# Performance work log

Hardware: AMD Instinct MI355X
Metric: run time of the kernel (lower is better)

## Reference

```python
import jax, jax.numpy as jnp
import numpy as np

B, H, W = 16, 32, 32
N = H * W
C_SEARCH, C_XCORR = 256, 64
C = C_SEARCH + C_XCORR          # phi_in_channels = gcn_in_channels
PHI_H = 64
GC_HID, GC_OUT = 128, 1
K_PTS = 48                       # keypoints per image
BN_EPS = 1e-5


def _build_coords_pair():
    # 8-neighbourhood pairs (distance^2 in {1,2}), exactly gen_8neigh_coords_pair
    idx = np.arange(N).reshape(H, W)
    ys, xs = np.meshgrid(np.arange(H), np.arange(W), indexing='ij')
    pairs8 = []
    for dy in (-1, 0, 1):
        for dx in (-1, 0, 1):
            if dy == 0 and dx == 0:
                continue
            ny, nx = ys + dy, xs + dx
            m = (ny >= 0) & (ny < H) & (nx >= 0) & (nx < W)
            pairs8.append(np.stack([idx[ys[m], xs[m]], idx[ny[m], nx[m]]], axis=1))
    pairs8 = np.concatenate(pairs8, 0)  # [7812, 2]
    # keypoint permutation pairs; keypoints on even coords -> disjoint from 8-neigh
    even = np.arange(0, H, 2)
    grid_idx = (even[:, None] * W + even[None, :]).reshape(-1)
    rng = np.random.default_rng(0)
    out = []
    for _ in range(B):
        kp = rng.choice(grid_idx, size=K_PTS, replace=False)
        a, b = np.meshgrid(kp, kp, indexing='ij')
        m = a != b
        kpairs = np.stack([a[m], b[m]], axis=1)  # K*(K-1) ordered pairs
        out.append(np.concatenate([kpairs, pairs8], 0))
    return np.stack(out, 0).astype(np.int32)  # [B, E, 2]


def setup_inputs() -> dict:
    key = jax.random.key(0)
    ks = jax.random.split(key, 10)
    u = lambda k, shape, s: jax.random.uniform(k, shape, jnp.float32, -s, s)
    inp = {
        'search_feature': jax.random.normal(ks[0], (B, C_SEARCH, H, W), jnp.float32),
        'xcorr_map': jax.random.normal(ks[1], (B, C_XCORR, H, W), jnp.float32),
        'coords_pair': jnp.asarray(_build_coords_pair()),
        # phi: Linear(C, PHI_H) + BN + ReLU, then Linear(PHI_H, 1) + Sigmoid
        'phi_w1': u(ks[2], (C, PHI_H), 1.0 / np.sqrt(C)),
        'phi_b1': u(ks[3], (PHI_H,), 1.0 / np.sqrt(C)),
        'bn_gamma': jnp.ones((PHI_H,), jnp.float32),
        'bn_beta': jnp.zeros((PHI_H,), jnp.float32),
        'phi_w2': u(ks[4], (PHI_H, 1), 1.0 / np.sqrt(PHI_H)),
        'phi_b2': u(ks[5], (1,), 1.0 / np.sqrt(PHI_H)),
        # GCN weights, torch init: uniform(-1/sqrt(out), 1/sqrt(out))
        'gc1_w': u(ks[6], (C, GC_HID), 1.0 / np.sqrt(GC_HID)),
        'gc2_w': u(ks[7], (GC_HID, GC_OUT), 1.0 / np.sqrt(GC_OUT)),
    }
    return inp


def reference(search_feature, xcorr_map, coords_pair, phi_w1, phi_b1,
              bn_gamma, bn_beta, phi_w2, phi_b2, gc1_w, gc2_w):
    # catted feature flattened: [B, C, N] (row-major h*W+w, matches torch view)
    feat = jnp.concatenate([search_feature, xcorr_map], axis=1).reshape(B, C, N)

    def per_image(f, pairs):  # f: [C, N], pairs: [E, 2]
        diff = jnp.abs(f[:, pairs[:, 0]] - f[:, pairs[:, 1]]).T  # [E, C]
        h = diff @ phi_w1 + phi_b1                                # [E, PHI_H]
        mu = jnp.mean(h, axis=0)
        var = jnp.var(h, axis=0)  # biased, as torch BN training mode
        h = (h - mu) / jnp.sqrt(var + BN_EPS) * bn_gamma + bn_beta
        h = jax.nn.relu(h)
        edge = jax.nn.sigmoid(h @ phi_w2 + phi_b2)[:, 0]          # [E]
        adj = jnp.zeros((N, N), jnp.float32).at[pairs[:, 0], pairs[:, 1]].set(edge)
        return adj

    adj = jax.vmap(per_image)(feat, coords_pair)  # [B, N, N]

    node_feat = feat.transpose(0, 2, 1)  # [B, N, C] (gcn_process_feat_xcorr=True)
    h = jax.nn.leaky_relu(jnp.einsum('bnm,bmd->bnd', adj, node_feat @ gc1_w), 0.2)
    mask = jax.nn.sigmoid(jnp.einsum('bnm,bmd->bnd', adj, h @ gc2_w))  # [B, N, 1]
    return mask[:, :, 0].reshape(B, 1, H, W)
```

## Files before the change

kernel.cpp:

```cpp
#include <hip/hip_runtime.h>
#include <hip/hip_bf16.h>
#include <hip/hip_fp16.h>

#define BB 16
#define NN 1024
#define CS 256
#define CX 64
#define CC 320
#define PH 64
#define GH 128
#define ELLW 64
#define NENG 7812
#define ROWP 324
#define RSTR 164
#define NKPH 1128
#define NGU  3906
#define NUD  5034

typedef __hip_bfloat16 bf16;
typedef __attribute__((ext_vector_type(8))) __bf16 bfrag;
typedef __attribute__((ext_vector_type(4))) float v4f;

__device__ __forceinline__ void tri_decode(int m, int& a, int& y) {
    float s = sqrtf((float)(9025 - 8 * m));
    int aa = (int)((95.0f - s) * 0.5f);
    if (aa > 0 && 47 * aa - (aa * (aa - 1)) / 2 > m) --aa;
    while (47 * (aa + 1) - ((aa + 1) * aa) / 2 <= m) ++aa;
    a = aa;
    y = aa + 1 + (m - (47 * aa - (aa * (aa - 1)) / 2));
}

__global__ __launch_bounds__(256) void k_prep_transpose(
    const float* __restrict__ search, const float* __restrict__ xcorr,
    float* __restrict__ featT,
    const float* __restrict__ w1, const float* __restrict__ gc1w,
    __bf16* __restrict__ whi, __bf16* __restrict__ wlo,
    __bf16* __restrict__ gwhi, __bf16* __restrict__ gwlo,
    int* __restrict__ cnt, float* __restrict__ Ssum, float* __restrict__ S2sum)
{
    __shared__ float tile[32][33];
    int blk = blockIdx.x;
    int tid = threadIdx.x;
    if (blk < BB * 320) {
        int b   = blk % BB;
        int rem = blk / BB;
        int ct  = rem >> 5;
        int ntl = rem & 31;
        int cl = tid >> 5, nl = tid & 31;
        const float* sb = search + (size_t)b * CS * NN;
        const float* xb = xcorr + (size_t)b * CX * NN;
        #pragma unroll
        for (int f = 0; f < 4; ++f) {
            int c = ct * 32 + cl + f * 8;
            int n = ntl * 32 + nl;
            float v = (c < CS) ? sb[(size_t)c * NN + n] : xb[(size_t)(c - CS) * NN + n];
            tile[cl + f * 8][nl] = v;
        }
        __syncthreads();
        #pragma unroll
        for (int f = 0; f < 4; ++f) {
            int nr = cl + f * 8;
            int cc = nl;
            featT[((size_t)b * NN + ntl * 32 + nr) * CC + ct * 32 + cc] = tile[cc][nr];
        }
    } else {
        int idx = (blk - BB * 320) * 256 + tid;
        if (idx < 10 * 4 * 64 * 8) {
            int j    = idx & 7;
            int lane = (idx >> 3) & 63;
            int nt   = (idx >> 9) & 3;
            int ks   = idx >> 11;
            int k = ks * 32 + (lane >> 4) * 8 + j;
            int n = nt * 16 + (lane & 15);
            float w = w1[k * PH + n];
            __bf16 h = (__bf16)w;
            whi[idx] = h;
            wlo[idx] = (__bf16)(w - (float)h);
        }
        if (idx < 10 * 8 * 64 * 8) {
            int j    = idx & 7;
            int lane = (idx >> 3) & 63;
            int nt   = (idx >> 9) & 7;
            int ks   = idx >> 12;
            int k = ks * 32 + (lane >> 4) * 8 + j;
            int n = nt * 16 + (lane & 15);
            float w = gc1w[k * GH + n];
            __bf16 h = (__bf16)w;
            gwhi[idx] = h;
            gwlo[idx] = (__bf16)(w - (float)h);
        }
        if (idx < BB * NN) cnt[idx] = 0;
        if (idx < BB * PH) { Ssum[idx] = 0.f; S2sum[idx] = 0.f; }
    }
}

__global__ __launch_bounds__(256, 2) void k_edge(
    const float* __restrict__ featT, const int* __restrict__ pairs,
    const __bf16* __restrict__ wglob, const float* __restrict__ b1,
    bf16* __restrict__ hstore, float* __restrict__ Ssum,
    float* __restrict__ S2sum, int E, int EKP)
{
    __shared__ float RowsBuf[15552];
    __shared__ int kpn[48];

    int t = threadIdx.x;
    int wave = t >> 6, lane = t & 63;
    int q = lane >> 4, r = lane & 15;
    int b = blockIdx.x % BB;
    int y = blockIdx.x / BB;

    if (t < 48) kpn[t] = pairs[((size_t)b * E + t * 47) * 2];

    const bfrag* WH = (const bfrag*)wglob;
    const bfrag* WL = WH + 2560;

    float b1v[4];
    #pragma unroll
    for (int nt = 0; nt < 4; ++nt) b1v[nt] = b1[nt * 16 + r];
    float ps[4], ps2[4];
    #pragma unroll
    for (int nt = 0; nt < 4; ++nt) { ps[nt] = 0.f; ps2[nt] = 0.f; }

    const int dyT[4] = {-1,-1,-1, 0};
    const int dxT[4] = {-1, 0, 1,-1};
    const int pfT4[4] = {0, 961, 1953, 2914};

    int d = wave;
    int dy = dyT[d], dx = dxT[d];
    int y0 = dy < 0 ? 1 : 0;
    int x0 = dx < 0 ? 1 : 0;
    int ww = (dx == 0) ? 32 : 31;
    int pfF = pfT4[d];

    const float* rowI[2];
    const float* rowJ[2];
    #pragma unroll
    for (int mt = 0; mt < 2; ++mt) {
        int x  = (mt << 4) + r;
        int ni = 32 + x;
        int xj = x + dx; xj = xj < 0 ? 0 : (xj > 31 ? 31 : xj);
        int nj = (1 + dy) * 32 + xj;
        rowI[mt] = &RowsBuf[ni * RSTR + q * 8];
        rowJ[mt] = &RowsBuf[nj * RSTR + q * 8];
    }

    v4f acc[2][4];
    #pragma unroll
    for (int mt = 0; mt < 2; ++mt)
        #pragma unroll
        for (int nt = 0; nt < 4; ++nt) acc[mt][nt] = (v4f)0.f;

    #pragma unroll
    for (int ph = 0; ph < 2; ++ph) {
        __syncthreads();
        const int ch0 = ph * 160;
        #pragma unroll
        for (int k = 0; k < 10; ++k) {
            int uu = t + k * 256;
            int node = uu / 40, c4 = uu - node * 40;
            int gy = y - 1 + (node >> 5);
            if (gy >= 0) {
                int gn = gy * 32 + (node & 31);
                float4 v = *(const float4*)&featT[((size_t)b * NN + gn) * CC
                                                  + ch0 + c4 * 4];
                *(float4*)&RowsBuf[node * RSTR + c4 * 4] = v;
            }
        }
        __syncthreads();

        const int ksBeg = ph * 5;
        #pragma unroll
        for (int ks = ksBeg; ks < ksBeg + 5; ++ks) {
            int lc = ks * 32 - ch0;
            #pragma unroll
            for (int mt = 0; mt < 2; ++mt) {
                float4 fi0 = *(const float4*)(rowI[mt] + lc);
                float4 fi1 = *(const float4*)(rowI[mt] + lc + 4);
                float4 fj0 = *(const float4*)(rowJ[mt] + lc);
                float4 fj1 = *(const float4*)(rowJ[mt] + lc + 4);
                float df[8];
                df[0] = fabsf(fi0.x - fj0.x); df[1] = fabsf(fi0.y - fj0.y);
                df[2] = fabsf(fi0.z - fj0.z); df[3] = fabsf(fi0.w - fj0.w);
                df[4] = fabsf(fi1.x - fj1.x); df[5] = fabsf(fi1.y - fj1.y);
                df[6] = fabsf(fi1.z - fj1.z); df[7] = fabsf(fi1.w - fj1.w);

                bfrag ah, al;
                #pragma unroll
                for (int kk = 0; kk < 8; ++kk) {
                    __bf16 h = (__bf16)df[kk];
                    ah[kk] = h;
                    al[kk] = (__bf16)(df[kk] - (float)h);
                }
                #pragma unroll
                for (int nt = 0; nt < 4; ++nt) {
                    bfrag bh = WH[((ks * 4 + nt) << 6) + lane];
                    bfrag bl = WL[((ks * 4 + nt) << 6) + lane];
                    acc[mt][nt] = __builtin_amdgcn_mfma_f32_16x16x32_bf16(
                        ah, bh, acc[mt][nt], 0, 0, 0);
                    acc[mt][nt] = __builtin_amdgcn_mfma_f32_16x16x32_bf16(
                        ah, bl, acc[mt][nt], 0, 0, 0);
                    acc[mt][nt] = __builtin_amdgcn_mfma_f32_16x16x32_bf16(
                        al, bh, acc[mt][nt], 0, 0, 0);
                }
            }
        }
    }

    __syncthreads();
    {
        const float4* src = (const float4*)featT;
        #pragma unroll
        for (int k = 0; k < 15; ++k) {
            int idx = t + k * 256;
            int slot = idx / 80, c4 = idx - slot * 80;
            float4 v = src[((size_t)b * NN + kpn[slot]) * 80 + c4];
            *(float4*)&RowsBuf[slot * ROWP + c4 * 4] = v;
        }
    }

    #pragma unroll
    for (int mt = 0; mt < 2; ++mt) {
        #pragma unroll
        for (int reg = 0; reg < 4; ++reg) {
            int xi = (mt << 4) + q * 4 + reg;
            int y2 = y + dy, x2 = xi + dx;
            bool valid = ((unsigned)y2 < 32u) && ((unsigned)x2 < 32u);
            if (valid) {
                int e1 = EKP + pfF + (y - y0) * ww + (xi - x0);
                bf16* h1 = hstore + ((size_t)b * E + e1) * PH + r;
                #pragma unroll
                for (int nt = 0; nt < 4; ++nt) {
                    float v = acc[mt][nt][reg] + b1v[nt];
                    h1[nt * 16] = __float2bfloat16(v);
                    ps[nt] += v;
                    ps2[nt] = fmaf(v, v, ps2[nt]);
                }
            }
        }
    }

    __syncthreads();

    int u = y + 32 * wave;
    if (u < 71) {
        int mA = u * 16 + r;
        if (mA >= NKPH) mA = NKPH - 1;
        int aI, yI;
        tri_decode(mA, aI, yI);
        const float* rI = &RowsBuf[aI * ROWP + q * 8];
        const float* rJ = &RowsBuf[yI * ROWP + q * 8];

        v4f acc2[4];
        #pragma unroll
        for (int nt = 0; nt < 4; ++nt) acc2[nt] = (v4f)0.f;

        #pragma unroll
        for (int ks = 0; ks < 10; ++ks) {
            float4 fi0 = *(const float4*)(rI + ks * 32);
            float4 fi1 = *(const float4*)(rI + ks * 32 + 4);
            float4 fj0 = *(const float4*)(rJ + ks * 32);
            float4 fj1 = *(const float4*)(rJ + ks * 32 + 4);
            float df[8];
            df[0] = fabsf(fi0.x - fj0.x); df[1] = fabsf(fi0.y - fj0.y);
            df[2] = fabsf(fi0.z - fj0.z); df[3] = fabsf(fi0.w - fj0.w);
            df[4] = fabsf(fi1.x - fj1.x); df[5] = fabsf(fi1.y - fj1.y);
            df[6] = fabsf(fi1.z - fj1.z); df[7] = fabsf(fi1.w - fj1.w);

            bfrag ah, al;
            #pragma unroll
            for (int kk = 0; kk < 8; ++kk) {
                __bf16 h = (__bf16)df[kk];
                ah[kk] = h;
                al[kk] = (__bf16)(df[kk] - (float)h);
            }
            #pragma unroll
            for (int nt = 0; nt < 4; ++nt) {
                bfrag bh = WH[((ks * 4 + nt) << 6) + lane];
                bfrag bl = WL[((ks * 4 + nt) << 6) + lane];
                acc2[nt] = __builtin_amdgcn_mfma_f32_16x16x32_bf16(ah, bh, acc2[nt], 0, 0, 0);
                acc2[nt] = __builtin_amdgcn_mfma_f32_16x16x32_bf16(ah, bl, acc2[nt], 0, 0, 0);
                acc2[nt] = __builtin_amdgcn_mfma_f32_16x16x32_bf16(al, bh, acc2[nt], 0, 0, 0);
            }
        }

        #pragma unroll
        for (int reg = 0; reg < 4; ++reg) {
            int mC = u * 16 + q * 4 + reg;
            if (mC < NKPH) {
                int a, yk;
                tri_decode(mC, a, yk);
                int e1 = a * 47 + yk - 1;
                bf16* h1 = hstore + ((size_t)b * E + e1) * PH + r;
                #pragma unroll
                for (int nt = 0; nt < 4; ++nt) {
                    float v = acc2[nt][reg] + b1v[nt];
                    h1[nt * 16] = __float2bfloat16(v);
                    ps[nt] += v;
                    ps2[nt] = fmaf(v, v, ps2[nt]);
                }
            }
        }
    }

    __syncthreads();
    float* sS  = RowsBuf;
    float* sS2 = RowsBuf + PH;
    if (t < PH) { sS[t] = 0.f; sS2[t] = 0.f; }
    __syncthreads();
    #pragma unroll
    for (int nt = 0; nt < 4; ++nt) {
        float p1 = ps[nt]  + __shfl_xor(ps[nt], 16, 64);
        p1 += __shfl_xor(p1, 32, 64);
        float p2 = ps2[nt] + __shfl_xor(ps2[nt], 16, 64);
        p2 += __shfl_xor(p2, 32, 64);
        if (lane < 16) {
            atomicAdd(&sS[nt * 16 + r],  2.0f * p1);
            atomicAdd(&sS2[nt * 16 + r], 2.0f * p2);
        }
    }
    __syncthreads();
    if (t < PH) {
        atomicAdd(&Ssum[b * PH + t],  sS[t]);
        atomicAdd(&S2sum[b * PH + t], sS2[t]);
    }
}

__global__ __launch_bounds__(256, 2) void k_val_gc1(
    const float* __restrict__ featT, const __bf16* __restrict__ gwhi,
    const __bf16* __restrict__ gwlo, __half* __restrict__ g1,
    const bf16* __restrict__ hstore, const float* __restrict__ Ssum,
    const float* __restrict__ S2sum, const float* __restrict__ gamma,
    const float* __restrict__ beta, const float* __restrict__ w2,
    const float* __restrict__ b2, const int* __restrict__ pairs,
    int* __restrict__ cnt, int* __restrict__ ecol, float* __restrict__ eval_,
    int E, int EKP, int nGC)
{
    __shared__ ushort WG[40960];

    int t = threadIdx.x;
    if ((int)blockIdx.x < nGC) {
        int b = blockIdx.x % BB;
        int rem = blockIdx.x / BB;
        int half = rem & 1;
        int m0 = b * NN + (rem >> 1) * 64;

        {
            uint4* dst = (uint4*)WG;
            const uint4* sh = (const uint4*)gwhi;
            const uint4* sl = (const uint4*)gwlo;
            #pragma unroll
            for (int k = 0; k < 10; ++k) {
                int u = t + k * 256;
                int chunk = u >> 6, v = u & 63;
                int ks = chunk >> 2, ntp = chunk & 3;
                int src = (ks * 8 + half * 4 + ntp) * 64 + v;
                dst[u]        = sh[src];
                dst[2560 + u] = sl[src];
            }
        }

        int wave = t >> 6, lane = t & 63;
        int q = lane >> 4, r = lane & 15;
        const float* fp = featT + (size_t)(m0 + wave * 16 + r) * CC + q * 8;

        float fa[2][8];
        auto LOADA = [&](int ks, int buf) {
            const float4* p = (const float4*)(fp + ks * 32);
            *(float4*)&fa[buf][0] = p[0];
            *(float4*)&fa[buf][4] = p[1];
        };

        v4f acc[4];
        #pragma unroll
        for (int nt = 0; nt < 4; ++nt) acc[nt] = (v4f)0.f;

        LOADA(0, 0);
        __syncthreads();

        const bfrag* WGH = (const bfrag*)WG;
        const bfrag* WGL = (const bfrag*)(WG + 20480);

        #pragma unroll
        for (int ks = 0; ks < 10; ++ks) {
            int cur = ks & 1;
            if (ks < 9) LOADA(ks + 1, cur ^ 1);
            bfrag ah, al;
            #pragma unroll
            for (int kk = 0; kk < 8; ++kk) {
                float d = fa[cur][kk];
                __bf16 h = (__bf16)d;
                ah[kk] = h;
                al[kk] = (__bf16)(d - (float)h);
            }
            #pragma unroll
            for (int nt = 0; nt < 4; ++nt) {
                bfrag bh = WGH[((ks * 4 + nt) << 6) + lane];
                bfrag bl = WGL[((ks * 4 + nt) << 6) + lane];
                acc[nt] = __builtin_amdgcn_mfma_f32_16x16x32_bf16(ah, bh, acc[nt], 0, 0, 0);
                acc[nt] = __builtin_amdgcn_mfma_f32_16x16x32_bf16(ah, bl, acc[nt], 0, 0, 0);
                acc[nt] = __builtin_amdgcn_mfma_f32_16x16x32_bf16(al, bh, acc[nt], 0, 0, 0);
            }
        }
        #pragma unroll
        for (int nt = 0; nt < 4; ++nt) {
            #pragma unroll
            for (int reg = 0; reg < 4; ++reg) {
                int m = m0 + wave * 16 + q * 4 + reg;
                g1[(size_t)m * GH + (half * 4 + nt) * 16 + r] =
                    __float2half(acc[nt][reg]);
            }
        }
    } else {
        float* ca = (float*)WG;
        float* cb = ca + PH;
        int* kpl = (int*)(cb + PH);
        int blk = blockIdx.x - nGC;
        int b = blk % BB;
        int u = (blk / BB) * 256 + t;
        if (t < PH) {
            int l = t;
            float mu = Ssum[b * PH + l] / E;
            float var = S2sum[b * PH + l] / E - mu * mu;
            float A = rsqrtf(var + 1e-5f) * gamma[l];
            ca[l] = A;
            cb[l] = beta[l] - mu * A;
        }
        if (t < 48) kpl[t] = pairs[((size_t)b * E + t * 47) * 2];
        __syncthreads();
        if (u >= NUD) return;

        int i, j, hrow;
        if (u < NKPH) {
            int a, yk;
            tri_decode(u, a, yk);
            i = kpl[a]; j = kpl[yk];
            hrow = a * 47 + yk - 1;
        } else {
            int up = u - NKPH;
            int pf, ww, y0, x0, dy, dx;
            if (up < 961)       { pf = 0;    ww = 31; y0 = 1; x0 = 1; dy = -1; dx = -1; }
            else if (up < 1953) { pf = 961;  ww = 32; y0 = 1; x0 = 0; dy = -1; dx = 0;  }
            else if (up < 2914) { pf = 1953; ww = 31; y0 = 1; x0 = 0; dy = -1; dx = 1;  }
            else                { pf = 2914; ww = 31; y0 = 0; x0 = 1; dy = 0;  dx = -1; }
            int rel = up - pf;
            int yR = rel / ww, xC = rel - yR * ww;
            int yy = yR + y0, xi = xC + x0;
            i = yy * 32 + xi;
            j = (yy + dy) * 32 + (xi + dx);
            hrow = EKP + up;
        }

        const bfrag* hp = (const bfrag*)(hstore + ((size_t)b * E + hrow) * PH);
        float acc = 0.f;
        #pragma unroll
        for (int l8 = 0; l8 < 8; ++l8) {
            bfrag hv = hp[l8];
            #pragma unroll
            for (int c = 0; c < 8; ++c) {
                int l = l8 * 8 + c;
                float x = fmaf((float)hv[c], ca[l], cb[l]);
                x = x > 0.f ? x : 0.f;
                acc = fmaf(x, w2[l], acc);
            }
        }
        float edge = 1.f / (1.f + __expf(-(acc + b2[0])));
        int ri = b * NN + i;
        int rj = b * NN + j;
        int s1 = atomicAdd(&cnt[ri], 1);
        if (s1 < ELLW) {
            ecol[ri * ELLW + s1]  = j;
            eval_[ri * ELLW + s1] = edge;
        }
        int s2 = atomicAdd(&cnt[rj], 1);
        if (s2 < ELLW) {
            ecol[rj * ELLW + s2]  = i;
            eval_[rj * ELLW + s2] = edge;
        }
    }
}

__global__ __launch_bounds__(256) void k_spmm1(
    const __half* __restrict__ g1, const int* __restrict__ cnt,
    const int* __restrict__ ecol, const float* __restrict__ eval_,
    const float* __restrict__ w2g, float* __restrict__ g2)
{
    int tid = threadIdx.x & 63;
    int node = blockIdx.x * 4 + (threadIdx.x >> 6);
    int base = node & ~(NN - 1);
    float wa = w2g[2 * tid], wb = w2g[2 * tid + 1];
    int c = cnt[node];
    const int* ec = ecol + (size_t)node * ELLW;
    const float* ev = eval_ + (size_t)node * ELLW;
    const __half2* g1v = (const __half2*)g1;
    float aa = 0.f, ab = 0.f;
    int s = 0;
    for (; s + 4 <= c; s += 4) {
        int j0 = ec[s], j1 = ec[s + 1], j2 = ec[s + 2], j3 = ec[s + 3];
        float v0 = ev[s], v1 = ev[s + 1], v2 = ev[s + 2], v3 = ev[s + 3];
        __half2 u0 = g1v[((size_t)(base + j0)) * 64 + tid];
        __half2 u1 = g1v[((size_t)(base + j1)) * 64 + tid];
        __half2 u2 = g1v[((size_t)(base + j2)) * 64 + tid];
        __half2 u3 = g1v[((size_t)(base + j3)) * 64 + tid];
        aa = fmaf(v0, __low2float(u0), aa); ab = fmaf(v0, __high2float(u0), ab);
        aa = fmaf(v1, __low2float(u1), aa); ab = fmaf(v1, __high2float(u1), ab);
        aa = fmaf(v2, __low2float(u2), aa); ab = fmaf(v2, __high2float(u2), ab);
        aa = fmaf(v3, __low2float(u3), aa); ab = fmaf(v3, __high2float(u3), ab);
    }
    for (; s < c; ++s) {
        __half2 u = g1v[((size_t)(base + ec[s])) * 64 + tid];
        float v = ev[s];
        aa = fmaf(v, __low2float(u), aa); ab = fmaf(v, __high2float(u), ab);
    }
    float h1a = aa > 0.f ? aa : 0.2f * aa;
    float h1b = ab > 0.f ? ab : 0.2f * ab;
    float p = h1a * wa + h1b * wb;
    #pragma unroll
    for (int off = 32; off >= 1; off >>= 1) p += __shfl_down(p, off, 64);
    if (tid == 0) g2[node] = p;
}

__global__ __launch_bounds__(256) void k_spmm2(
    const float* __restrict__ g2, const int* __restrict__ cnt,
    const int* __restrict__ ecol, const float* __restrict__ eval_,
    float* __restrict__ out)
{
    int lane = threadIdx.x & 63;
    int node = blockIdx.x * 4 + (threadIdx.x >> 6);
    int base = node & ~(NN - 1);
    int c = cnt[node];
    float p = 0.f;
    if (lane < c) {
        int j = ecol[(size_t)node * ELLW + lane];
        p = eval_[(size_t)node * ELLW + lane] * g2[base + j];
    }
    #pragma unroll
    for (int off = 32; off >= 1; off >>= 1) p += __shfl_down(p, off, 64);
    if (lane == 0) out[node] = 1.f / (1.f + __expf(-p));
}

extern "C" void kernel_launch(void* const* d_in, const int* in_sizes, int n_in,
                              void* d_out, int out_size, void* d_ws, size_t ws_size,
                              hipStream_t stream)
{
    const float* search = (const float*)d_in[0];
    const float* xcorr  = (const float*)d_in[1];
    const int*   pairs  = (const int*)d_in[2];
    const float* w1     = (const float*)d_in[3];
    const float* b1     = (const float*)d_in[4];
    const float* gamma  = (const float*)d_in[5];
    const float* beta   = (const float*)d_in[6];
    const float* w2     = (const float*)d_in[7];
    const float* b2     = (const float*)d_in[8];
    const float* gc1w   = (const float*)d_in[9];
    const float* gc2w   = (const float*)d_in[10];
    float* out = (float*)d_out;

    int E   = in_sizes[2] / (BB * 2);
    int EKP = E - NENG;
    int nbU  = (NUD + 255) / 256;
    int nGC  = BB * 32;

    char* ws = (char*)d_ws;
    size_t off = 0;
    auto alloc = [&](size_t bytes) {
        size_t o = off;
        off += (bytes + 255) & ~(size_t)255;
        return o;
    };
    __bf16* whi   = (__bf16*)(ws + alloc(10 * 4 * 64 * 8 * 2));
    __bf16* wlo   = (__bf16*)(ws + alloc(10 * 4 * 64 * 8 * 2));
    __bf16* gwhi  = (__bf16*)(ws + alloc(10 * 8 * 64 * 8 * 2));
    __bf16* gwlo  = (__bf16*)(ws + alloc(10 * 8 * 64 * 8 * 2));
    float* featT  = (float*)(ws + alloc((size_t)BB * NN * CC * 4));
    bf16*  hstore = (bf16*)(ws + alloc((size_t)BB * E * PH * 2));
    float* Ssum   = (float*)(ws + alloc(BB * PH * 4));
    float* S2sum  = (float*)(ws + alloc(BB * PH * 4));
    int*   cnt    = (int*)(ws + alloc(BB * NN * 4));
    int*   ecol   = (int*)(ws + alloc((size_t)BB * NN * ELLW * 4));
    float* eval_  = (float*)(ws + alloc((size_t)BB * NN * ELLW * 4));
    __half* g1    = (__half*)(ws + alloc((size_t)BB * NN * GH * 2));
    float* g2     = (float*)(ws + alloc(BB * NN * 4));
    (void)ws_size; (void)n_in; (void)out_size;

    k_prep_transpose<<<dim3(BB * 320 + 160), dim3(256), 0, stream>>>(
        search, xcorr, featT, w1, gc1w, whi, wlo, gwhi, gwlo, cnt, Ssum, S2sum);
    k_edge<<<dim3(BB * 32), dim3(256), 0, stream>>>(featT, pairs, whi, b1,
                                                    hstore, Ssum, S2sum,
                                                    E, EKP);
    k_val_gc1<<<dim3(nGC + BB * nbU), dim3(256), 0, stream>>>(
        featT, gwhi, gwlo, g1, hstore, Ssum, S2sum, gamma, beta, w2, b2,
        pairs, cnt, ecol, eval_, E, EKP, nGC);
    k_spmm1<<<dim3(BB * NN / 4), dim3(256), 0, stream>>>(g1, cnt, ecol, eval_,
                                                         gc2w, g2);
    k_spmm2<<<dim3(BB * NN / 4), dim3(256), 0, stream>>>(g2, cnt, ecol, eval_, out);
}
```

Before: 149.0 us.

## Split edge kernel into many small blocks reading features directly from global memory

Reworks k_edge so it no longer stages neighbour rows and keypoint rows in a large shared buffer. Each wave now computes one 16-edge tile, reading its operands straight from featT in global memory. The grid is split into 1024 neighbour blocks plus 288 keypoint blocks instead of 512 blocks, and launch bounds rise to 4 blocks per CU. This is meant to raise occupancy and parallelism and to remove the shared-memory staging and its barriers, at the cost of redundant global/L2 reads of feature rows.

```diff
diff --git a/kernel.cpp b/kernel.cpp
--- a/kernel.cpp
+++ b/kernel.cpp
@@ -11,8 +11,6 @@
 #define GH 128
 #define ELLW 64
 #define NENG 7812
-#define ROWP 324
-#define RSTR 164
 #define NKPH 1128
 #define NGU  3906
 #define NUD  5034
@@ -94,22 +92,18 @@
     }
 }
 
-__global__ __launch_bounds__(256, 2) void k_edge(
+__global__ __launch_bounds__(256, 4) void k_edge(
     const float* __restrict__ featT, const int* __restrict__ pairs,
     const __bf16* __restrict__ wglob, const float* __restrict__ b1,
     bf16* __restrict__ hstore, float* __restrict__ Ssum,
     float* __restrict__ S2sum, int E, int EKP)
 {
-    __shared__ float RowsBuf[15552];
-    __shared__ int kpn[48];
+    __shared__ float sS[PH];
+    __shared__ float sS2[PH];
 
     int t = threadIdx.x;
     int wave = t >> 6, lane = t & 63;
     int q = lane >> 4, r = lane & 15;
-    int b = blockIdx.x % BB;
-    int y = blockIdx.x / BB;
-
-    if (t < 48) kpn[t] = pairs[((size_t)b * E + t * 47) * 2];
 
     const bfrag* WH = (const bfrag*)wglob;
     const bfrag* WL = WH + 2560;
@@ -120,64 +114,107 @@
     float ps[4], ps2[4];
     #pragma unroll
     for (int nt = 0; nt < 4; ++nt) { ps[nt] = 0.f; ps2[nt] = 0.f; }
-
-    const int dyT[4] = {-1,-1,-1, 0};
-    const int dxT[4] = {-1, 0, 1,-1};
-    const int pfT4[4] = {0, 961, 1953, 2914};
-
-    int d = wave;
-    int dy = dyT[d], dx = dxT[d];
-    int y0 = dy < 0 ? 1 : 0;
-    int x0 = dx < 0 ? 1 : 0;
-    int ww = (dx == 0) ? 32 : 31;
-    int pfF = pfT4[d];
-
-    const float* rowI[2];
-    const float* rowJ[2];
-    #pragma unroll
-    for (int mt = 0; mt < 2; ++mt) {
-        int x  = (mt << 4) + r;
-        int ni = 32 + x;
-        int xj = x + dx; xj = xj < 0 ? 0 : (xj > 31 ? 31 : xj);
-        int nj = (1 + dy) * 32 + xj;
-        rowI[mt] = &RowsBuf[ni * RSTR + q * 8];
-        rowJ[mt] = &RowsBuf[nj * RSTR + q * 8];
-    }
-
-    v4f acc[2][4];
-    #pragma unroll
-    for (int mt = 0; mt < 2; ++mt)
-        #pragma unroll
-        for (int nt = 0; nt < 4; ++nt) acc[mt][nt] = (v4f)0.f;
-
-    #pragma unroll
-    for (int ph = 0; ph < 2; ++ph) {
-        __syncthreads();
-        const int ch0 = ph * 160;
-        #pragma unroll
-        for (int k = 0; k < 10; ++k) {
-            int uu = t + k * 256;
-            int node = uu / 40, c4 = uu - node * 40;
-            int gy = y - 1 + (node >> 5);
-            if (gy >= 0) {
-                int gn = gy * 32 + (node & 31);
-                float4 v = *(const float4*)&featT[((size_t)b * NN + gn) * CC
-                                                  + ch0 + c4 * 4];
-                *(float4*)&RowsBuf[node * RSTR + c4 * 4] = v;
-            }
-        }
-        __syncthreads();
-
-        const int ksBeg = ph * 5;
-        #pragma unroll
-        for (int ks = ksBeg; ks < ksBeg + 5; ++ks) {
-            int lc = ks * 32 - ch0;
-            #pragma unroll
-            for (int mt = 0; mt < 2; ++mt) {
-                float4 fi0 = *(const float4*)(rowI[mt] + lc);
-                float4 fi1 = *(const float4*)(rowI[mt] + lc + 4);
-                float4 fj0 = *(const float4*)(rowJ[mt] + lc);
-                float4 fj1 = *(const float4*)(rowJ[mt] + lc + 4);
+    int b;
+
+    if (blockIdx.x < 1024) {
+        int blk = blockIdx.x;
+        b = blk >> 6;
+        int rb = blk & 63;
+        int mt = rb >> 5;
+        int d  = (rb >> 3) & 3;
+        int y  = ((rb & 7) << 2) + wave;
+
+        const int dyT[4] = {-1,-1,-1, 0};
+        const int dxT[4] = {-1, 0, 1,-1};
+        const int pfT4[4] = {0, 961, 1953, 2914};
+        int dy = dyT[d], dx = dxT[d];
+        int y0 = dy < 0 ? 1 : 0;
+        int x0 = dx < 0 ? 1 : 0;
+        int ww = (dx == 0) ? 32 : 31;
+        int pfF = pfT4[d];
+
+        int xiL = mt * 16 + r;
+        int ni = y * 32 + xiL;
+        int xj = xiL + dx; xj = xj < 0 ? 0 : (xj > 31 ? 31 : xj);
+        int gy = y + dy; int gyc = gy < 0 ? 0 : gy;
+        int nj = gyc * 32 + xj;
+        const float* rI = featT + ((size_t)b * NN + ni) * CC + q * 8;
+        const float* rJ = featT + ((size_t)b * NN + nj) * CC + q * 8;
+
+        v4f acc[4];
+        #pragma unroll
+        for (int nt = 0; nt < 4; ++nt) acc[nt] = (v4f)0.f;
+
+        #pragma unroll
+        for (int ks = 0; ks < 10; ++ks) {
+            float4 fi0 = *(const float4*)(rI + ks * 32);
+            float4 fi1 = *(const float4*)(rI + ks * 32 + 4);
+            float4 fj0 = *(const float4*)(rJ + ks * 32);
+            float4 fj1 = *(const float4*)(rJ + ks * 32 + 4);
+            float df[8];
+            df[0] = fabsf(fi0.x - fj0.x); df[1] = fabsf(fi0.y - fj0.y);
+            df[2] = fabsf(fi0.z - fj0.z); df[3] = fabsf(fi0.w - fj0.w);
+            df[4] = fabsf(fi1.x - fj1.x); df[5] = fabsf(fi1.y - fj1.y);
+            df[6] = fabsf(fi1.z - fj1.z); df[7] = fabsf(fi1.w - fj1.w);
+
+            bfrag ah, al;
+            #pragma unroll
+            for (int kk = 0; kk < 8; ++kk) {
+                __bf16 h = (__bf16)df[kk];
+                ah[kk] = h;
+                al[kk] = (__bf16)(df[kk] - (float)h);
+            }
+            #pragma unroll
+            for (int nt = 0; nt < 4; ++nt) {
+                bfrag bh = WH[((ks * 4 + nt) << 6) + lane];
+                bfrag bl = WL[((ks * 4 + nt) << 6) + lane];
+                acc[nt] = __builtin_amdgcn_mfma_f32_16x16x32_bf16(ah, bh, acc[nt], 0, 0, 0);
+                acc[nt] = __builtin_amdgcn_mfma_f32_16x16x32_bf16(ah, bl, acc[nt], 0, 0, 0);
+                acc[nt] = __builtin_amdgcn_mfma_f32_16x16x32_bf16(al, bh, acc[nt], 0, 0, 0);
+            }
+        }
+
+        #pragma unroll
+        for (int reg = 0; reg < 4; ++reg) {
+            int xi = mt * 16 + q * 4 + reg;
+            int y2 = y + dy, x2 = xi + dx;
+            bool valid = ((unsigned)y2 < 32u) && ((unsigned)x2 < 32u);
+            if (valid) {
+                int e1 = EKP + pfF + (y - y0) * ww + (xi - x0);
+                bf16* h1 = hstore + ((size_t)b * E + e1) * PH + r;
+                #pragma unroll
+                for (int nt = 0; nt < 4; ++nt) {
+                    float v = acc[nt][reg] + b1v[nt];
+                    h1[nt * 16] = __float2bfloat16(v);
+                    ps[nt] += v;
+                    ps2[nt] = fmaf(v, v, ps2[nt]);
+                }
+            }
+        }
+    } else {
+        int kblk = blockIdx.x - 1024;
+        b = kblk / 18;
+        int u = (kblk % 18) * 4 + wave;
+        if (u < 71) {
+            int mA = u * 16 + r;
+            if (mA >= NKPH) mA = NKPH - 1;
+            int aI, yI;
+            tri_decode(mA, aI, yI);
+            int na = pairs[((size_t)b * E + aI * 47) * 2];
+            int ny = pairs[((size_t)b * E + yI * 47) * 2];
+            const float* rI = featT + ((size_t)b * NN + na) * CC + q * 8;
+            const float* rJ = featT + ((size_t)b * NN + ny) * CC + q * 8;
+
+            v4f acc2[4];
+            #pragma unroll
+            for (int nt = 0; nt < 4; ++nt) acc2[nt] = (v4f)0.f;
+
+            #pragma unroll
+            for (int ks = 0; ks < 10; ++ks) {
+                float4 fi0 = *(const float4*)(rI + ks * 32);
+                float4 fi1 = *(const float4*)(rI + ks * 32 + 4);
+                float4 fj0 = *(const float4*)(rJ + ks * 32);
+                float4 fj1 = *(const float4*)(rJ + ks * 32 + 4);
                 float df[8];
                 df[0] = fabsf(fi0.x - fj0.x); df[1] = fabsf(fi0.y - fj0.y);
                 df[2] = fabsf(fi0.z - fj0.z); df[3] = fabsf(fi0.w - fj0.w);
@@ -195,116 +232,32 @@
                 for (int nt = 0; nt < 4; ++nt) {
                     bfrag bh = WH[((ks * 4 + nt) << 6) + lane];
                     bfrag bl = WL[((ks * 4 + nt) << 6) + lane];
-                    acc[mt][nt] = __builtin_amdgcn_mfma_f32_16x16x32_bf16(
-                        ah, bh, acc[mt][nt], 0, 0, 0);
-                    acc[mt][nt] = __builtin_amdgcn_mfma_f32_16x16x32_bf16(
-                        ah, bl, acc[mt][nt], 0, 0, 0);
-                    acc[mt][nt] = __builtin_amdgcn_mfma_f32_16x16x32_bf16(
-                        al, bh, acc[mt][nt], 0, 0, 0);
+                    acc2[nt] = __builtin_amdgcn_mfma_f32_16x16x32_bf16(ah, bh, acc2[nt], 0, 0, 0);
+                    acc2[nt] = __builtin_amdgcn_mfma_f32_16x16x32_bf16(ah, bl, acc2[nt], 0, 0, 0);
+                    acc2[nt] = __builtin_amdgcn_mfma_f32_16x16x32_bf16(al, bh, acc2[nt], 0, 0, 0);
                 }
             }
-        }
-    }
-
-    __syncthreads();
-    {
-        const float4* src = (const float4*)featT;
-        #pragma unroll
-        for (int k = 0; k < 15; ++k) {
-            int idx = t + k * 256;
-            int slot = idx / 80, c4 = idx - slot * 80;
-            float4 v = src[((size_t)b * NN + kpn[slot]) * 80 + c4];
-            *(float4*)&RowsBuf[slot * ROWP + c4 * 4] = v;
-        }
-    }
-
-    #pragma unroll
-    for (int mt = 0; mt < 2; ++mt) {
-        #pragma unroll
-        for (int reg = 0; reg < 4; ++reg) {
-            int xi = (mt << 4) + q * 4 + reg;
-            int y2 = y + dy, x2 = xi + dx;
-            bool valid = ((unsigned)y2 < 32u) && ((unsigned)x2 < 32u);
-            if (valid) {
-                int e1 = EKP + pfF + (y - y0) * ww + (xi - x0);
-                bf16* h1 = hstore + ((size_t)b * E + e1) * PH + r;
-                #pragma unroll
-                for (int nt = 0; nt < 4; ++nt) {
-                    float v = acc[mt][nt][reg] + b1v[nt];
-                    h1[nt * 16] = __float2bfloat16(v);
-                    ps[nt] += v;
-                    ps2[nt] = fmaf(v, v, ps2[nt]);
+
+            #pragma unroll
+            for (int reg = 0; reg < 4; ++reg) {
+                int mC = u * 16 + q * 4 + reg;
+                if (mC < NKPH) {
+                    int a, yk;
+                    tri_decode(mC, a, yk);
+                    int e1 = a * 47 + yk - 1;
+                    bf16* h1 = hstore + ((size_t)b * E + e1) * PH + r;
+                    #pragma unroll
+                    for (int nt = 0; nt < 4; ++nt) {
+                        float v = acc2[nt][reg] + b1v[nt];
+                        h1[nt * 16] = __float2bfloat16(v);
+                        ps[nt] += v;
+                        ps2[nt] = fmaf(v, v, ps2[nt]);
+                    }
                 }
             }
         }
     }
 
-    __syncthreads();
-
-    int u = y + 32 * wave;
-    if (u < 71) {
-        int mA = u * 16 + r;
-        if (mA >= NKPH) mA = NKPH - 1;
-        int aI, yI;
-        tri_decode(mA, aI, yI);
-        const float* rI = &RowsBuf[aI * ROWP + q * 8];
-        const float* rJ = &RowsBuf[yI * ROWP + q * 8];
-
-        v4f acc2[4];
-        #pragma unroll
-        for (int nt = 0; nt < 4; ++nt) acc2[nt] = (v4f)0.f;
-
-        #pragma unroll
-        for (int ks = 0; ks < 10; ++ks) {
-            float4 fi0 = *(const float4*)(rI + ks * 32);
-            float4 fi1 = *(const float4*)(rI + ks * 32 + 4);
-            float4 fj0 = *(const float4*)(rJ + ks * 32);
-            float4 fj1 = *(const float4*)(rJ + ks * 32 + 4);
-            float df[8];
-            df[0] = fabsf(fi0.x - fj0.x); df[1] = fabsf(fi0.y - fj0.y);
-            df[2] = fabsf(fi0.z - fj0.z); df[3] = fabsf(fi0.w - fj0.w);
-            df[4] = fabsf(fi1.x - fj1.x); df[5] = fabsf(fi1.y - fj1.y);
-            df[6] = fabsf(fi1.z - fj1.z); df[7] = fabsf(fi1.w - fj1.w);
-
-            bfrag ah, al;
-            #pragma unroll
-            for (int kk = 0; kk < 8; ++kk) {
-                __bf16 h = (__bf16)df[kk];
-                ah[kk] = h;
-                al[kk] = (__bf16)(df[kk] - (float)h);
-            }
-            #pragma unroll
-            for (int nt = 0; nt < 4; ++nt) {
-                bfrag bh = WH[((ks * 4 + nt) << 6) + lane];
-                bfrag bl = WL[((ks * 4 + nt) << 6) + lane];
-                acc2[nt] = __builtin_amdgcn_mfma_f32_16x16x32_bf16(ah, bh, acc2[nt], 0, 0, 0);
-                acc2[nt] = __builtin_amdgcn_mfma_f32_16x16x32_bf16(ah, bl, acc2[nt], 0, 0, 0);
-                acc2[nt] = __builtin_amdgcn_mfma_f32_16x16x32_bf16(al, bh, acc2[nt], 0, 0, 0);
-            }
-        }
-
-        #pragma unroll
-        for (int reg = 0; reg < 4; ++reg) {
-            int mC = u * 16 + q * 4 + reg;
-            if (mC < NKPH) {
-                int a, yk;
-                tri_decode(mC, a, yk);
-                int e1 = a * 47 + yk - 1;
-                bf16* h1 = hstore + ((size_t)b * E + e1) * PH + r;
-                #pragma unroll
-                for (int nt = 0; nt < 4; ++nt) {
-                    float v = acc2[nt][reg] + b1v[nt];
-                    h1[nt * 16] = __float2bfloat16(v);
-                    ps[nt] += v;
-                    ps2[nt] = fmaf(v, v, ps2[nt]);
-                }
-            }
-        }
-    }
-
-    __syncthreads();
-    float* sS  = RowsBuf;
-    float* sS2 = RowsBuf + PH;
     if (t < PH) { sS[t] = 0.f; sS2[t] = 0.f; }
     __syncthreads();
     #pragma unroll
@@ -584,9 +537,9 @@
 
     k_prep_transpose<<<dim3(BB * 320 + 160), dim3(256), 0, stream>>>(
         search, xcorr, featT, w1, gc1w, whi, wlo, gwhi, gwlo, cnt, Ssum, S2sum);
-    k_edge<<<dim3(BB * 32), dim3(256), 0, stream>>>(featT, pairs, whi, b1,
-                                                    hstore, Ssum, S2sum,
-                                                    E, EKP);
+    k_edge<<<dim3(1024 + BB * 18), dim3(256), 0, stream>>>(featT, pairs, whi, b1,
+                                                           hstore, Ssum, S2sum,
+                                                           E, EKP);
     k_val_gc1<<<dim3(nGC + BB * nbU), dim3(256), 0, stream>>>(
         featT, gwhi, gwlo, g1, hstore, Ssum, S2sum, gamma, beta, w2, b2,
         pairs, cnt, ecol, eval_, E, EKP, nGC);
```

New measurement: 172.1 us. +15.5%, slower.
